# Kernel optimization log

Measured on AMD Instinct MI355X. Metric: run time of the kernel, lower is better.

## Reference

```python
import jax, jax.numpy as jnp
import numpy as np

H = 1024          # hidden_size
V = 50257         # output vocab
L_ENC = 128       # encoder max_length
STEPS = 32        # loop_length
STOP = 658        # stop_id


def setup_inputs() -> dict:
    key = jax.random.key(0)
    ks = jax.random.split(key, 10)
    def w(k, shape, fan):
        return (jax.random.normal(k, shape, jnp.float32) / np.sqrt(fan)).astype(jnp.float32)
    return {
        "decoder_input": jnp.zeros((1,), jnp.int32),                     # SOS token = 0
        "decoder_hidden": jax.random.normal(ks[0], (1, H), jnp.float32),
        "encoder_outputs": jax.random.normal(ks[1], (L_ENC, H), jnp.float32),
        "embedding": w(ks[2], (V, H), H),
        "attn_w": w(ks[3], (L_ENC, 2 * H), 2 * H), "attn_b": jnp.zeros((L_ENC,), jnp.float32),
        "comb_w": w(ks[4], (H, 2 * H), 2 * H),     "comb_b": jnp.zeros((H,), jnp.float32),
        "gru_wih": w(ks[5], (3 * H, H), H), "gru_whh": w(ks[6], (3 * H, H), H),
        "gru_bih": jnp.zeros((3 * H,), jnp.float32), "gru_bhh": jnp.zeros((3 * H,), jnp.float32),
        "out_w": w(ks[7], (V, H), H), "out_b": jnp.zeros((V,), jnp.float32),
    }


def reference(decoder_input, decoder_hidden, encoder_outputs, embedding,
              attn_w, attn_b, comb_w, comb_b,
              gru_wih, gru_whh, gru_bih, gru_bhh, out_w, out_b):
    """Greedy attention-GRU decode; returns int32 ids [STEPS] (0 after stop)."""

    def step(carry, _):
        tok, h, done = carry                      # tok: [1] int32, h: [1,H], done: bool scalar
        emb = embedding[tok]                      # [1,H]  (dropout = identity in eval)
        # attention over encoder positions
        attn_logits = jnp.concatenate([emb, h], axis=1) @ attn_w.T + attn_b   # [1,L_ENC]
        aw = jax.nn.softmax(attn_logits, axis=1)
        ctx = aw @ encoder_outputs                # [1,H]
        x = jax.nn.relu(jnp.concatenate([emb, ctx], axis=1) @ comb_w.T + comb_b)  # [1,H]
        # one GRU step (PyTorch gate ordering: r, z, n)
        gi = x @ gru_wih.T + gru_bih              # [1,3H]
        gh = h @ gru_whh.T + gru_bhh
        ir, iz, inn = jnp.split(gi, 3, axis=1)
        hr, hz, hn = jnp.split(gh, 3, axis=1)
        r = jax.nn.sigmoid(ir + hr)
        z = jax.nn.sigmoid(iz + hz)
        n = jnp.tanh(inn + r * hn)
        h_new = (1.0 - z) * n + z * h             # [1,H]
        logits = h_new @ out_w.T + out_b          # [1,V]
        top = jnp.argmax(logits, axis=1).astype(jnp.int32)   # [1] greedy token
        out_id = jnp.where(done, jnp.zeros_like(top), top)   # ids after break stay 0
        done_new = done | (top[0] == 1) | (top[0] == STOP)
        h_next = jnp.where(done, h, h_new)
        return (top, h_next, done_new), out_id[0]

    init = (decoder_input, decoder_hidden, jnp.asarray(False))
    _, ids = jax.lax.scan(step, init, None, length=STEPS)
    return ids
```

## Files before the change

kernel.cpp:

```cpp
#include <hip/hip_runtime.h>
#include <hip/hip_bf16.h>
#include <math.h>

#define H 1024
#define L_ENC 128
#define V 50257
#define STEPS 32
#define STOP_ID 658

#define WS_H     0
#define WS_HNEW  1024
#define WS_GH    2048
#define WS_ALOG  5120
#define WS_X     5248
#define WS_PMAX  6272
#define WS_PIDX  6784
#define WS_TOK   7296
#define WS_DONE  7297

#define NB_OUT 508

__global__ __launch_bounds__(1024) void k_init(const int* __restrict__ dec_in,
                                               const float* __restrict__ h0,
                                               float* __restrict__ ws) {
    int t = threadIdx.x;
    ws[WS_H + t] = h0[t];
    if (t == 0) {
        ((int*)(ws + WS_TOK))[0]  = dec_in[0];
        ((int*)(ws + WS_DONE))[0] = 0;
    }
}

__global__ __launch_bounds__(256) void k_pre(const float* __restrict__ embedding,
                                             const float* __restrict__ attn_w,
                                             const float* __restrict__ attn_b,
                                             const float* __restrict__ whh,
                                             const float* __restrict__ bhh,
                                             float* __restrict__ ws) {
    const int wave = threadIdx.x >> 6, lane = threadIdx.x & 63;
    const int tok = ((const int*)(ws + WS_TOK))[0];
    const float4* h4 = (const float4*)(ws + WS_H);
    if (blockIdx.x < 32) {
        const int r = blockIdx.x * 4 + wave;
        const float4* w4 = (const float4*)(attn_w + (size_t)r * 2048);
        const float4* e4 = (const float4*)(embedding + (size_t)tok * H);
        float s = 0.f;
        for (int m = 0; m < 8; ++m) {
            int j = lane + (m << 6);
            float4 a = w4[j];
            float4 c = (j < 256) ? e4[j] : h4[j - 256];
            s += a.x * c.x + a.y * c.y + a.z * c.z + a.w * c.w;
        }
        for (int o = 32; o; o >>= 1) s += __shfl_down(s, o);
        if (lane == 0) ws[WS_ALOG + r] = s + attn_b[r];
    } else {
        const int r = (blockIdx.x - 32) * 4 + wave;
        const float4* w4 = (const float4*)(whh + (size_t)r * H);
        float s = 0.f;
        for (int m = 0; m < 4; ++m) {
            int j = lane + (m << 6);
            float4 a = w4[j], b = h4[j];
            s += a.x * b.x + a.y * b.y + a.z * b.z + a.w * b.w;
        }
        for (int o = 32; o; o >>= 1) s += __shfl_down(s, o);
        if (lane == 0) ws[WS_GH + r] = s + bhh[r];
    }
}

__global__ __launch_bounds__(256) void k_ctx_comb(const float* __restrict__ embedding,
                                                  const float* __restrict__ enc,
                                                  const float* __restrict__ comb_w,
                                                  const float* __restrict__ comb_b,
                                                  float* __restrict__ ws) {
    __shared__ float s_aw[L_ENC];
    __shared__ __align__(16) float s_cat[2048];
    const int t = threadIdx.x;
    const int tok = ((const int*)(ws + WS_TOK))[0];

    if (t < L_ENC) s_aw[t] = ws[WS_ALOG + t];
    __syncthreads();
    float mx = -INFINITY;
    for (int l = 0; l < L_ENC; ++l) mx = fmaxf(mx, s_aw[l]);
    __syncthreads();
    if (t < L_ENC) s_aw[t] = expf(s_aw[t] - mx);
    __syncthreads();
    float ssum = 0.f;
    for (int l = 0; l < L_ENC; ++l) ssum += s_aw[l];
    const float inv = 1.f / ssum;

    float4* cat4 = (float4*)s_cat;
    const float4* e4   = (const float4*)(embedding + (size_t)tok * H);
    const float4* enc4 = (const float4*)enc;
    cat4[t] = e4[t];
    float4 c = make_float4(0.f, 0.f, 0.f, 0.f);
    for (int l = 0; l < L_ENC; ++l) {
        float a = s_aw[l];
        float4 e = enc4[l * 256 + t];
        c.x += a * e.x; c.y += a * e.y; c.z += a * e.z; c.w += a * e.w;
    }
    cat4[256 + t] = make_float4(c.x * inv, c.y * inv, c.z * inv, c.w * inv);
    __syncthreads();

    const int wave = t >> 6, lane = t & 63;
    for (int k = 0; k < 4; ++k) {
        const int r = blockIdx.x * 16 + wave * 4 + k;
        const float4* w4 = (const float4*)(comb_w + (size_t)r * 2048);
        float s = 0.f;
        for (int m = 0; m < 8; ++m) {
            int j = lane + (m << 6);
            float4 a = w4[j], b = cat4[j];
            s += a.x * b.x + a.y * b.y + a.z * b.z + a.w * b.w;
        }
        for (int o = 32; o; o >>= 1) s += __shfl_down(s, o);
        if (lane == 0) ws[WS_X + r] = fmaxf(s + comb_b[r], 0.f);
    }
}

__global__ __launch_bounds__(256) void k_gru(const float* __restrict__ wih,
                                             const float* __restrict__ bih,
                                             float* __restrict__ ws) {
    __shared__ __align__(16) float s_x[H];
    const int t = threadIdx.x, wave = t >> 6, lane = t & 63;
    for (int j = t; j < H; j += 256) s_x[j] = ws[WS_X + j];
    __syncthreads();
    const float4* x4 = (const float4*)s_x;
    const int i = blockIdx.x * 4 + wave;
    float g[3];
    for (int p = 0; p < 3; ++p) {
        const float4* w4 = (const float4*)(wih + (size_t)(i + p * H) * H);
        float s = 0.f;
        for (int m = 0; m < 4; ++m) {
            int j = lane + (m << 6);
            float4 a = w4[j], b = x4[j];
            s += a.x * b.x + a.y * b.y + a.z * b.z + a.w * b.w;
        }
        for (int o = 32; o; o >>= 1) s += __shfl_down(s, o);
        g[p] = s;
    }
    if (lane == 0) {
        float gr = g[0] + bih[i]         + ws[WS_GH + i];
        float gz = g[1] + bih[i + H]     + ws[WS_GH + i + H];
        float gn = g[2] + bih[i + 2*H];
        float r = 1.f / (1.f + expf(-gr));
        float z = 1.f / (1.f + expf(-gz));
        float n = tanhf(gn + r * ws[WS_GH + i + 2*H]);
        ws[WS_HNEW + i] = (1.f - z) * n + z * ws[WS_H + i];
    }
}

__global__ __launch_bounds__(256) void k_logits(const float* __restrict__ out_w,
                                                const float* __restrict__ out_b,
                                                float* __restrict__ ws) {
    __shared__ __align__(16) float s_h[H];
    __shared__ float s_bv[4];
    __shared__ int   s_bi[4];
    const int t = threadIdx.x, wave = t >> 6, lane = t & 63;
    for (int j = t; j < H; j += 256) s_h[j] = ws[WS_HNEW + j];
    __syncthreads();
    const float4* h4 = (const float4*)s_h;
    const int base = blockIdx.x * 99;
    const int end  = min(base + 99, V);
    float bv = -INFINITY; int bi = 0x7fffffff;
    for (int r0 = base + wave; r0 < end; r0 += 4) {
        const float4* w4 = (const float4*)(out_w + (size_t)r0 * H);
        float s = 0.f;
        for (int m = 0; m < 4; ++m) {
            int j = lane + (m << 6);
            float4 a = w4[j], b = h4[j];
            s += a.x * b.x + a.y * b.y + a.z * b.z + a.w * b.w;
        }
        for (int o = 32; o; o >>= 1) s += __shfl_xor(s, o);
        s += out_b[r0];
        if (s > bv) { bv = s; bi = r0; }
    }
    if (lane == 0) { s_bv[wave] = bv; s_bi[wave] = bi; }
    __syncthreads();
    if (t == 0) {
        for (int w2 = 1; w2 < 4; ++w2) {
            float v = s_bv[w2]; int i2 = s_bi[w2];
            if (v > bv || (v == bv && i2 < bi)) { bv = v; bi = i2; }
        }
        ws[WS_PMAX + blockIdx.x] = bv;
        ((int*)(ws + WS_PIDX))[blockIdx.x] = bi;
    }
}

__global__ __launch_bounds__(512) void k_reduce(float* __restrict__ ws,
                                                int* __restrict__ out, int step) {
    __shared__ float s_v[512];
    __shared__ int   s_i[512];
    __shared__ int   s_done;
    const int t = threadIdx.x;
    s_v[t] = (t < NB_OUT) ? ws[WS_PMAX + t] : -INFINITY;
    s_i[t] = (t < NB_OUT) ? ((int*)(ws + WS_PIDX))[t] : 0x7fffffff;
    if (t == 0) s_done = ((int*)(ws + WS_DONE))[0];
    __syncthreads();
    for (int o = 256; o; o >>= 1) {
        if (t < o) {
            float v2 = s_v[t + o]; int i2 = s_i[t + o];
            if (v2 > s_v[t] || (v2 == s_v[t] && i2 < s_i[t])) { s_v[t] = v2; s_i[t] = i2; }
        }
        __syncthreads();
    }
    const int top = s_i[0];
    const int done_old = s_done;
    if (!done_old) {
        ws[WS_H + t]       = ws[WS_HNEW + t];
        ws[WS_H + t + 512] = ws[WS_HNEW + t + 512];
    }
    if (t == 0) {
        out[step] = done_old ? 0 : top;
        ((int*)(ws + WS_TOK))[0]  = top;
        ((int*)(ws + WS_DONE))[0] = done_old | (top == 1) | (top == STOP_ID);
    }
}

extern "C" void kernel_launch(void* const* d_in, const int* in_sizes, int n_in,
                              void* d_out, int out_size, void* d_ws, size_t ws_size,
                              hipStream_t stream) {
    const int*   dec_in = (const int*)  d_in[0];
    const float* h0     = (const float*)d_in[1];
    const float* enc    = (const float*)d_in[2];
    const float* emb    = (const float*)d_in[3];
    const float* attn_w = (const float*)d_in[4];
    const float* attn_b = (const float*)d_in[5];
    const float* comb_w = (const float*)d_in[6];
    const float* comb_b = (const float*)d_in[7];
    const float* wih    = (const float*)d_in[8];
    const float* whh    = (const float*)d_in[9];
    const float* bih    = (const float*)d_in[10];
    const float* bhh    = (const float*)d_in[11];
    const float* out_w  = (const float*)d_in[12];
    const float* out_b  = (const float*)d_in[13];
    float* ws = (float*)d_ws;
    int*   out = (int*)d_out;

    k_init<<<1, 1024, 0, stream>>>(dec_in, h0, ws);
    for (int step = 0; step < STEPS; ++step) {
        k_pre<<<800, 256, 0, stream>>>(emb, attn_w, attn_b, whh, bhh, ws);
        k_ctx_comb<<<64, 256, 0, stream>>>(emb, enc, comb_w, comb_b, ws);
        k_gru<<<256, 256, 0, stream>>>(wih, bih, ws);
        k_logits<<<NB_OUT, 256, 0, stream>>>(out_w, out_b, ws);
        k_reduce<<<1, 512, 0, stream>>>(ws, out, step);
    }
}
```

Baseline: 2.933 ms.

## Fuse attention into comb kernel, fold argmax reduce into logits via last-block atomic

Merges the attention-logit, softmax/context, combine and W_hh matvecs into a single launch. Each of the 64 comb blocks now recomputes the full 128 attention logits redundantly, and the other blocks compute gh. The final argmax reduction moves into the last-finishing logits block using an atomic counter and threadfence, which removes one launch per step. Matvec loops are restructured to issue all weight loads up front and to compute several rows per wave, raising memory-level parallelism. The trade-offs are redundant attn_w reads and a serialized tail in the last block.

```diff
diff --git a/kernel.cpp b/kernel.cpp
--- a/kernel.cpp
+++ b/kernel.cpp
@@ -11,14 +11,15 @@
 #define WS_H     0
 #define WS_HNEW  1024
 #define WS_GH    2048
-#define WS_ALOG  5120
-#define WS_X     5248
-#define WS_PMAX  6272
+#define WS_X     5120
+#define WS_PMAX  6144
 #define WS_PIDX  6784
-#define WS_TOK   7296
-#define WS_DONE  7297
-
-#define NB_OUT 508
+#define WS_TOK   7424
+#define WS_DONE  7425
+#define WS_CNT   7426
+
+#define NB_OUT 629
+#define ROWS_PB 80
 
 __global__ __launch_bounds__(1024) void k_init(const int* __restrict__ dec_in,
                                                const float* __restrict__ h0,
@@ -28,91 +29,120 @@
     if (t == 0) {
         ((int*)(ws + WS_TOK))[0]  = dec_in[0];
         ((int*)(ws + WS_DONE))[0] = 0;
-    }
-}
-
-__global__ __launch_bounds__(256) void k_pre(const float* __restrict__ embedding,
-                                             const float* __restrict__ attn_w,
-                                             const float* __restrict__ attn_b,
-                                             const float* __restrict__ whh,
-                                             const float* __restrict__ bhh,
-                                             float* __restrict__ ws) {
-    const int wave = threadIdx.x >> 6, lane = threadIdx.x & 63;
+        ((unsigned*)(ws + WS_CNT))[0] = 0;
+    }
+}
+
+__global__ __launch_bounds__(256) void k_A(const float* __restrict__ embedding,
+                                           const float* __restrict__ attn_w,
+                                           const float* __restrict__ attn_b,
+                                           const float* __restrict__ enc,
+                                           const float* __restrict__ comb_w,
+                                           const float* __restrict__ comb_b,
+                                           const float* __restrict__ whh,
+                                           const float* __restrict__ bhh,
+                                           float* __restrict__ ws) {
+    const int t = threadIdx.x, wave = t >> 6, lane = t & 63;
     const int tok = ((const int*)(ws + WS_TOK))[0];
-    const float4* h4 = (const float4*)(ws + WS_H);
-    if (blockIdx.x < 32) {
-        const int r = blockIdx.x * 4 + wave;
-        const float4* w4 = (const float4*)(attn_w + (size_t)r * 2048);
-        const float4* e4 = (const float4*)(embedding + (size_t)tok * H);
+    const float4* h4g = (const float4*)(ws + WS_H);
+
+    if (blockIdx.x >= 64) {
+        const int r = (blockIdx.x - 64) * 4 + wave;
+        const float4* w4 = (const float4*)(whh + (size_t)r * H);
+        float4 a[4], b[4];
+        #pragma unroll
+        for (int m = 0; m < 4; ++m) { a[m] = w4[lane + (m << 6)]; }
+        #pragma unroll
+        for (int m = 0; m < 4; ++m) { b[m] = h4g[lane + (m << 6)]; }
         float s = 0.f;
-        for (int m = 0; m < 8; ++m) {
-            int j = lane + (m << 6);
-            float4 a = w4[j];
-            float4 c = (j < 256) ? e4[j] : h4[j - 256];
-            s += a.x * c.x + a.y * c.y + a.z * c.z + a.w * c.w;
-        }
-        for (int o = 32; o; o >>= 1) s += __shfl_down(s, o);
-        if (lane == 0) ws[WS_ALOG + r] = s + attn_b[r];
-    } else {
-        const int r = (blockIdx.x - 32) * 4 + wave;
-        const float4* w4 = (const float4*)(whh + (size_t)r * H);
-        float s = 0.f;
-        for (int m = 0; m < 4; ++m) {
-            int j = lane + (m << 6);
-            float4 a = w4[j], b = h4[j];
-            s += a.x * b.x + a.y * b.y + a.z * b.z + a.w * b.w;
-        }
+        #pragma unroll
+        for (int m = 0; m < 4; ++m)
+            s += a[m].x * b[m].x + a[m].y * b[m].y + a[m].z * b[m].z + a[m].w * b[m].w;
+        #pragma unroll
         for (int o = 32; o; o >>= 1) s += __shfl_down(s, o);
         if (lane == 0) ws[WS_GH + r] = s + bhh[r];
-    }
-}
-
-__global__ __launch_bounds__(256) void k_ctx_comb(const float* __restrict__ embedding,
-                                                  const float* __restrict__ enc,
-                                                  const float* __restrict__ comb_w,
-                                                  const float* __restrict__ comb_b,
-                                                  float* __restrict__ ws) {
-    __shared__ float s_aw[L_ENC];
+        return;
+    }
+
+    __shared__ float s_alog[L_ENC];
+    __shared__ __align__(16) float s_eh[2048];
     __shared__ __align__(16) float s_cat[2048];
-    const int t = threadIdx.x;
-    const int tok = ((const int*)(ws + WS_TOK))[0];
-
-    if (t < L_ENC) s_aw[t] = ws[WS_ALOG + t];
-    __syncthreads();
+    const float4* e4 = (const float4*)(embedding + (size_t)tok * H);
+    float4* eh4  = (float4*)s_eh;
+    float4* cat4 = (float4*)s_cat;
+    float4 ev = e4[t];
+    eh4[t] = ev;
+    eh4[256 + t] = h4g[t];
+    cat4[t] = ev;
+    __syncthreads();
+
+    for (int it = 0; it < 16; ++it) {
+        const int r0 = wave * 32 + it * 2;
+        const float4* wa = (const float4*)(attn_w + (size_t)r0 * 2048);
+        float4 a0[8], a1[8];
+        #pragma unroll
+        for (int m = 0; m < 8; ++m) a0[m] = wa[lane + (m << 6)];
+        #pragma unroll
+        for (int m = 0; m < 8; ++m) a1[m] = wa[512 + lane + (m << 6)];
+        float s0 = 0.f, s1 = 0.f;
+        #pragma unroll
+        for (int m = 0; m < 8; ++m) {
+            float4 c = eh4[lane + (m << 6)];
+            s0 += a0[m].x * c.x + a0[m].y * c.y + a0[m].z * c.z + a0[m].w * c.w;
+            s1 += a1[m].x * c.x + a1[m].y * c.y + a1[m].z * c.z + a1[m].w * c.w;
+        }
+        #pragma unroll
+        for (int o = 32; o; o >>= 1) { s0 += __shfl_down(s0, o); s1 += __shfl_down(s1, o); }
+        if (lane == 0) {
+            s_alog[r0]     = s0 + attn_b[r0];
+            s_alog[r0 + 1] = s1 + attn_b[r0 + 1];
+        }
+    }
+    __syncthreads();
+
     float mx = -INFINITY;
-    for (int l = 0; l < L_ENC; ++l) mx = fmaxf(mx, s_aw[l]);
-    __syncthreads();
-    if (t < L_ENC) s_aw[t] = expf(s_aw[t] - mx);
+    #pragma unroll 4
+    for (int l = 0; l < L_ENC; ++l) mx = fmaxf(mx, s_alog[l]);
+    __syncthreads();
+    if (t < L_ENC) s_alog[t] = expf(s_alog[t] - mx);
     __syncthreads();
     float ssum = 0.f;
-    for (int l = 0; l < L_ENC; ++l) ssum += s_aw[l];
+    #pragma unroll 4
+    for (int l = 0; l < L_ENC; ++l) ssum += s_alog[l];
     const float inv = 1.f / ssum;
 
-    float4* cat4 = (float4*)s_cat;
-    const float4* e4   = (const float4*)(embedding + (size_t)tok * H);
     const float4* enc4 = (const float4*)enc;
-    cat4[t] = e4[t];
     float4 c = make_float4(0.f, 0.f, 0.f, 0.f);
+    #pragma unroll 4
     for (int l = 0; l < L_ENC; ++l) {
-        float a = s_aw[l];
+        float a = s_alog[l];
         float4 e = enc4[l * 256 + t];
         c.x += a * e.x; c.y += a * e.y; c.z += a * e.z; c.w += a * e.w;
     }
     cat4[256 + t] = make_float4(c.x * inv, c.y * inv, c.z * inv, c.w * inv);
     __syncthreads();
 
-    const int wave = t >> 6, lane = t & 63;
-    for (int k = 0; k < 4; ++k) {
-        const int r = blockIdx.x * 16 + wave * 4 + k;
-        const float4* w4 = (const float4*)(comb_w + (size_t)r * 2048);
-        float s = 0.f;
+    for (int it = 0; it < 2; ++it) {
+        const int r0 = blockIdx.x * 16 + wave * 4 + it * 2;
+        const float4* wc = (const float4*)(comb_w + (size_t)r0 * 2048);
+        float4 a0[8], a1[8];
+        #pragma unroll
+        for (int m = 0; m < 8; ++m) a0[m] = wc[lane + (m << 6)];
+        #pragma unroll
+        for (int m = 0; m < 8; ++m) a1[m] = wc[512 + lane + (m << 6)];
+        float s0 = 0.f, s1 = 0.f;
+        #pragma unroll
         for (int m = 0; m < 8; ++m) {
-            int j = lane + (m << 6);
-            float4 a = w4[j], b = cat4[j];
-            s += a.x * b.x + a.y * b.y + a.z * b.z + a.w * b.w;
-        }
-        for (int o = 32; o; o >>= 1) s += __shfl_down(s, o);
-        if (lane == 0) ws[WS_X + r] = fmaxf(s + comb_b[r], 0.f);
+            float4 b = cat4[lane + (m << 6)];
+            s0 += a0[m].x * b.x + a0[m].y * b.y + a0[m].z * b.z + a0[m].w * b.w;
+            s1 += a1[m].x * b.x + a1[m].y * b.y + a1[m].z * b.z + a1[m].w * b.w;
+        }
+        #pragma unroll
+        for (int o = 32; o; o >>= 1) { s0 += __shfl_down(s0, o); s1 += __shfl_down(s1, o); }
+        if (lane == 0) {
+            ws[WS_X + r0]     = fmaxf(s0 + comb_b[r0], 0.f);
+            ws[WS_X + r0 + 1] = fmaxf(s1 + comb_b[r0 + 1], 0.f);
+        }
     }
 }
 
@@ -125,22 +155,32 @@
     __syncthreads();
     const float4* x4 = (const float4*)s_x;
     const int i = blockIdx.x * 4 + wave;
-    float g[3];
-    for (int p = 0; p < 3; ++p) {
-        const float4* w4 = (const float4*)(wih + (size_t)(i + p * H) * H);
-        float s = 0.f;
-        for (int m = 0; m < 4; ++m) {
-            int j = lane + (m << 6);
-            float4 a = w4[j], b = x4[j];
-            s += a.x * b.x + a.y * b.y + a.z * b.z + a.w * b.w;
-        }
-        for (int o = 32; o; o >>= 1) s += __shfl_down(s, o);
-        g[p] = s;
+    const float4* w0 = (const float4*)(wih + (size_t)i * H);
+    const float4* w1 = (const float4*)(wih + (size_t)(i + H) * H);
+    const float4* w2 = (const float4*)(wih + (size_t)(i + 2 * H) * H);
+    float4 a0[4], a1[4], a2[4];
+    #pragma unroll
+    for (int m = 0; m < 4; ++m) a0[m] = w0[lane + (m << 6)];
+    #pragma unroll
+    for (int m = 0; m < 4; ++m) a1[m] = w1[lane + (m << 6)];
+    #pragma unroll
+    for (int m = 0; m < 4; ++m) a2[m] = w2[lane + (m << 6)];
+    float s0 = 0.f, s1 = 0.f, s2 = 0.f;
+    #pragma unroll
+    for (int m = 0; m < 4; ++m) {
+        float4 b = x4[lane + (m << 6)];
+        s0 += a0[m].x * b.x + a0[m].y * b.y + a0[m].z * b.z + a0[m].w * b.w;
+        s1 += a1[m].x * b.x + a1[m].y * b.y + a1[m].z * b.z + a1[m].w * b.w;
+        s2 += a2[m].x * b.x + a2[m].y * b.y + a2[m].z * b.z + a2[m].w * b.w;
+    }
+    #pragma unroll
+    for (int o = 32; o; o >>= 1) {
+        s0 += __shfl_down(s0, o); s1 += __shfl_down(s1, o); s2 += __shfl_down(s2, o);
     }
     if (lane == 0) {
-        float gr = g[0] + bih[i]         + ws[WS_GH + i];
-        float gz = g[1] + bih[i + H]     + ws[WS_GH + i + H];
-        float gn = g[2] + bih[i + 2*H];
+        float gr = s0 + bih[i]         + ws[WS_GH + i];
+        float gz = s1 + bih[i + H]     + ws[WS_GH + i + H];
+        float gn = s2 + bih[i + 2*H];
         float r = 1.f / (1.f + expf(-gr));
         float z = 1.f / (1.f + expf(-gz));
         float n = tanhf(gn + r * ws[WS_GH + i + 2*H]);
@@ -150,28 +190,52 @@
 
 __global__ __launch_bounds__(256) void k_logits(const float* __restrict__ out_w,
                                                 const float* __restrict__ out_b,
-                                                float* __restrict__ ws) {
+                                                float* __restrict__ ws,
+                                                int* __restrict__ out, int step) {
     __shared__ __align__(16) float s_h[H];
     __shared__ float s_bv[4];
     __shared__ int   s_bi[4];
+    __shared__ int   s_last;
+    __shared__ float s_rv[256];
+    __shared__ int   s_ri[256];
     const int t = threadIdx.x, wave = t >> 6, lane = t & 63;
     for (int j = t; j < H; j += 256) s_h[j] = ws[WS_HNEW + j];
     __syncthreads();
     const float4* h4 = (const float4*)s_h;
-    const int base = blockIdx.x * 99;
-    const int end  = min(base + 99, V);
+
+    const int rbase = blockIdx.x * ROWS_PB + wave * 20;
     float bv = -INFINITY; int bi = 0x7fffffff;
-    for (int r0 = base + wave; r0 < end; r0 += 4) {
-        const float4* w4 = (const float4*)(out_w + (size_t)r0 * H);
-        float s = 0.f;
+    for (int it = 0; it < 5; ++it) {
+        const int r = rbase + it * 4;
+        float4 a[4][4];
+        #pragma unroll
+        for (int q = 0; q < 4; ++q) {
+            const int rq = min(r + q, V - 1);
+            const float4* w4 = (const float4*)(out_w + (size_t)rq * H);
+            #pragma unroll
+            for (int m = 0; m < 4; ++m) a[q][m] = w4[lane + (m << 6)];
+        }
+        float s[4] = {0.f, 0.f, 0.f, 0.f};
+        #pragma unroll
         for (int m = 0; m < 4; ++m) {
-            int j = lane + (m << 6);
-            float4 a = w4[j], b = h4[j];
-            s += a.x * b.x + a.y * b.y + a.z * b.z + a.w * b.w;
-        }
-        for (int o = 32; o; o >>= 1) s += __shfl_xor(s, o);
-        s += out_b[r0];
-        if (s > bv) { bv = s; bi = r0; }
+            float4 b = h4[lane + (m << 6)];
+            #pragma unroll
+            for (int q = 0; q < 4; ++q)
+                s[q] += a[q][m].x * b.x + a[q][m].y * b.y + a[q][m].z * b.z + a[q][m].w * b.w;
+        }
+        #pragma unroll
+        for (int o = 32; o; o >>= 1) {
+            #pragma unroll
+            for (int q = 0; q < 4; ++q) s[q] += __shfl_xor(s[q], o);
+        }
+        #pragma unroll
+        for (int q = 0; q < 4; ++q) {
+            const int rq = r + q;
+            if (rq < V) {
+                float v = s[q] + out_b[rq];
+                if (v > bv) { bv = v; bi = rq; }
+            }
+        }
     }
     if (lane == 0) { s_bv[wave] = bv; s_bi[wave] = bi; }
     __syncthreads();
@@ -182,36 +246,41 @@
         }
         ws[WS_PMAX + blockIdx.x] = bv;
         ((int*)(ws + WS_PIDX))[blockIdx.x] = bi;
-    }
-}
-
-__global__ __launch_bounds__(512) void k_reduce(float* __restrict__ ws,
-                                                int* __restrict__ out, int step) {
-    __shared__ float s_v[512];
-    __shared__ int   s_i[512];
-    __shared__ int   s_done;
-    const int t = threadIdx.x;
-    s_v[t] = (t < NB_OUT) ? ws[WS_PMAX + t] : -INFINITY;
-    s_i[t] = (t < NB_OUT) ? ((int*)(ws + WS_PIDX))[t] : 0x7fffffff;
-    if (t == 0) s_done = ((int*)(ws + WS_DONE))[0];
-    __syncthreads();
-    for (int o = 256; o; o >>= 1) {
+        __threadfence();
+        unsigned prev = atomicAdd((unsigned*)(ws + WS_CNT), 1u);
+        s_last = (prev == NB_OUT - 1);
+    }
+    __syncthreads();
+    if (!s_last) return;
+
+    __threadfence();
+    volatile float* pv = ws + WS_PMAX;
+    volatile int*   pi = (int*)(ws + WS_PIDX);
+    float rv = -INFINITY; int ri = 0x7fffffff;
+    for (int e = t; e < NB_OUT; e += 256) {
+        float v = pv[e]; int i2 = pi[e];
+        if (v > rv || (v == rv && i2 < ri)) { rv = v; ri = i2; }
+    }
+    s_rv[t] = rv; s_ri[t] = ri;
+    __syncthreads();
+    #pragma unroll
+    for (int o = 128; o; o >>= 1) {
         if (t < o) {
-            float v2 = s_v[t + o]; int i2 = s_i[t + o];
-            if (v2 > s_v[t] || (v2 == s_v[t] && i2 < s_i[t])) { s_v[t] = v2; s_i[t] = i2; }
+            float v2 = s_rv[t + o]; int i2 = s_ri[t + o];
+            if (v2 > s_rv[t] || (v2 == s_rv[t] && i2 < s_ri[t])) { s_rv[t] = v2; s_ri[t] = i2; }
         }
         __syncthreads();
     }
-    const int top = s_i[0];
-    const int done_old = s_done;
+    const int top = s_ri[0];
+    const int done_old = ((const int*)(ws + WS_DONE))[0];
     if (!done_old) {
-        ws[WS_H + t]       = ws[WS_HNEW + t];
-        ws[WS_H + t + 512] = ws[WS_HNEW + t + 512];
+        for (int j = t; j < H; j += 256) ws[WS_H + j] = ws[WS_HNEW + j];
     }
     if (t == 0) {
         out[step] = done_old ? 0 : top;
         ((int*)(ws + WS_TOK))[0]  = top;
         ((int*)(ws + WS_DONE))[0] = done_old | (top == 1) | (top == STOP_ID);
+        ((unsigned*)(ws + WS_CNT))[0] = 0;
     }
 }
 
@@ -237,10 +306,8 @@
 
     k_init<<<1, 1024, 0, stream>>>(dec_in, h0, ws);
     for (int step = 0; step < STEPS; ++step) {
-        k_pre<<<800, 256, 0, stream>>>(emb, attn_w, attn_b, whh, bhh, ws);
-        k_ctx_comb<<<64, 256, 0, stream>>>(emb, enc, comb_w, comb_b, ws);
+        k_A<<<832, 256, 0, stream>>>(emb, attn_w, attn_b, enc, comb_w, comb_b, whh, bhh, ws);
         k_gru<<<256, 256, 0, stream>>>(wih, bih, ws);
-        k_logits<<<NB_OUT, 256, 0, stream>>>(out_w, out_b, ws);
-        k_reduce<<<1, 512, 0, stream>>>(ws, out, step);
-    }
-}
+        k_logits<<<NB_OUT, 256, 0, stream>>>(out_w, out_b, ws, out, step);
+    }
+}
```

Measured after the change: 3.727 ms. 1.27x slower.
